# Performance work log

Measured on AMD Instinct MI355X. Metric: run time of the kernel, lower is better.

## Reference

```python
import jax, jax.numpy as jnp
import numpy as np

B, C, H, W = 64, 2048, 14, 14
D, S, ITERS, EPS, HID = 256, 8, 3, 1e-8, 512


def build_pos(h, w, d):
    gy, gx = np.meshgrid(np.arange(h), np.arange(w), indexing='ij')
    q = d // 4
    omega = 1.0 / (10000.0 ** (np.arange(q) / q))
    ey = gy.reshape(-1, 1) * omega
    ex = gx.reshape(-1, 1) * omega
    pe = np.concatenate([np.sin(ey), np.cos(ey), np.sin(ex), np.cos(ex)], axis=1)
    return jnp.asarray(pe[None], jnp.float32)  # (1, h*w, d)


def layernorm(x, g, b, eps=1e-5):
    m = x.mean(-1, keepdims=True)
    v = ((x - m) ** 2).mean(-1, keepdims=True)
    return (x - m) * jax.lax.rsqrt(v + eps) * g + b


def setup_inputs() -> dict:
    key = jax.random.key(0)
    ks = jax.random.split(key, 16)
    w = lambda k, shp, s=0.02: jax.random.normal(k, shp, jnp.float32) * s
    inp = {
        'x': jax.random.normal(ks[0], (B, C, H, W), jnp.float32),
        'slot_noise': jax.random.normal(ks[1], (B, S, D), jnp.float32),
        'conv_w': w(ks[2], (C, D)), 'conv_b': jnp.zeros((D,), jnp.float32),
        'pos': build_pos(H, W, D),
        'slots_mu': jax.random.normal(ks[3], (1, 1, D), jnp.float32),
        'slots_logsigma': -jnp.ones((1, 1, D), jnp.float32),
        'qw': w(ks[4], (D, D)), 'qb': jnp.zeros((D,), jnp.float32),
        'kw': w(ks[5], (D, D)), 'kb': jnp.zeros((D,), jnp.float32),
        'vw': w(ks[6], (D, D)), 'vb': jnp.zeros((D,), jnp.float32),
        'gru_wih': w(ks[7], (D, 3 * D)), 'gru_whh': w(ks[8], (D, 3 * D)),
        'gru_bih': jnp.zeros((3 * D,), jnp.float32), 'gru_bhh': jnp.zeros((3 * D,), jnp.float32),
        'w1': w(ks[9], (D, HID)), 'b1': jnp.zeros((HID,), jnp.float32),
        'w2': w(ks[10], (HID, D)), 'b2': jnp.zeros((D,), jnp.float32),
        'ln_in_g': jnp.ones((D,), jnp.float32), 'ln_in_b': jnp.zeros((D,), jnp.float32),
        'ln_s_g': jnp.ones((D,), jnp.float32), 'ln_s_b': jnp.zeros((D,), jnp.float32),
        'ln_ff_g': jnp.ones((D,), jnp.float32), 'ln_ff_b': jnp.zeros((D,), jnp.float32),
    }
    return inp


def reference(x, slot_noise, conv_w, conv_b, pos, slots_mu, slots_logsigma,
              qw, qb, kw, kb, vw, vb, gru_wih, gru_whh, gru_bih, gru_bhh,
              w1, b1, w2, b2, ln_in_g, ln_in_b, ln_s_g, ln_s_b, ln_ff_g, ln_ff_b):
    b, c, h, w_ = x.shape
    d = qw.shape[0]
    scale = d ** (-0.5)
    # (B,C,H,W) -> (B,N,C) -> project -> add pos
    xt = x.transpose(0, 2, 3, 1).reshape(b, h * w_, c)
    xt = xt @ conv_w + conv_b + pos
    # slot init
    slots = slots_mu + jnp.exp(slots_logsigma) * slot_noise  # (B,S,D)
    inp = layernorm(xt, ln_in_g, ln_in_b)
    k = inp @ kw + kb
    v = inp @ vw + vb
    attn = None
    for _ in range(ITERS):
        slots_prev = slots
        s = layernorm(slots, ln_s_g, ln_s_b)
        q = s @ qw + qb
        dots = jnp.einsum('bid,bjd->bij', q, k) * scale  # (B,S,N)
        attn = jax.nn.softmax(dots, axis=1) + EPS  # softmax over slots
        attn = attn / attn.sum(-1, keepdims=True)  # renormalize over keys
        updates = jnp.einsum('bjd,bij->bid', v, attn)  # (B,S,D)
        # GRUCell (torch semantics)
        gi = updates @ gru_wih + gru_bih
        gh = slots_prev @ gru_whh + gru_bhh
        ir, iz, inn = jnp.split(gi, 3, axis=-1)
        hr, hz, hn = jnp.split(gh, 3, axis=-1)
        r = jax.nn.sigmoid(ir + hr)
        z = jax.nn.sigmoid(iz + hz)
        nn_ = jnp.tanh(inn + r * hn)
        slots = (1.0 - z) * nn_ + z * slots_prev
        ff = layernorm(slots, ln_ff_g, ln_ff_b)
        slots = slots + (jax.nn.relu(ff @ w1 + b1)) @ w2 + b2
    attn_map = attn.reshape(b, S, h, w_)
    return slots, attn_map
```

## Files before the change

kernel.cpp:

```cpp
#include <hip/hip_runtime.h>
#include <stdint.h>

#define HWN 196
#define CIN 2048
#define DD  256
#define BB  64
#define NSLOT 8
#define KVPAD 224
#define MTOT 12544

typedef __attribute__((ext_vector_type(8))) short short8;
typedef __attribute__((ext_vector_type(4))) float f32x4;
typedef __attribute__((ext_vector_type(4))) unsigned short us4;

__device__ __forceinline__ ushort f2bf(float f){ union{float f;uint32_t u;}v;v.f=f;uint32_t u=v.u;return (ushort)((u+0x7FFFu+((u>>16)&1u))>>16);}
__device__ __forceinline__ float bf2f(ushort h){ union{uint32_t u;float f;}v;v.u=((uint32_t)h)<<16;return v.f;}
__device__ __forceinline__ float sigm(float x){ return 1.f/(1.f+expf(-x)); }

__device__ __forceinline__ short8 ldsY(const ushort* buf, int LD, int kt, int lane){
    int row = lane & 15;
    int ch = kt*4 + (lane>>4);
    return *(const short8*)&buf[row*LD + ((ch ^ (row&7))<<3)];
}
__device__ __forceinline__ short8 gX(const ushort* base, int K, int nrow, int kt, int lane){
    return *(const short8*)&base[(size_t)nrow*K + kt*32 + (lane>>4)*8];
}

struct TD { const float* s; ushort* d; int R, C, t0; };
struct TD8 { TD a[8]; };

__global__ __launch_bounds__(256) void k_prep(TD8 td){
    __shared__ float tile[32][33];
    int bt = blockIdx.x;
    int mi = 0;
    #pragma unroll
    for (int i = 1; i < 8; ++i) if (bt >= td.a[i].t0) mi = i;
    TD d = td.a[mi];
    int lt = bt - d.t0;
    int tilesx = (d.C + 31) >> 5;
    int cb = (lt % tilesx) * 32, rb = (lt / tilesx) * 32;
    int tx = threadIdx.x & 31, ty = threadIdx.x >> 5;
    for (int i = ty; i < 32; i += 8) {
        int r = rb + i, c = cb + tx;
        tile[i][tx] = (r < d.R && c < d.C) ? d.s[(size_t)r * d.C + c] : 0.f;
    }
    __syncthreads();
    for (int i = ty; i < 32; i += 8) {
        int c = cb + i, r = rb + tx;
        if (c < d.C && r < d.R) d.d[(size_t)c * d.R + r] = f2bf(tile[tx][i]);
    }
}

__global__ __launch_bounds__(256) void k_proj(const float* __restrict__ x,
        const ushort* __restrict__ bT, const float* __restrict__ cb,
        const float* __restrict__ pos, ushort* __restrict__ xt){
    __shared__ ushort As[64 * 64];
    __shared__ ushort Bs[128 * 64];
    const int t = threadIdx.x;
    const int lane = t & 63;
    const int wv = t >> 6;
    const int wm = wv >> 1, wn = wv & 1;
    int mtile, nh;
    {
        int bid = blockIdx.x;
        if (bid < 384){
            int c = bid & 7, nhb = (bid >> 3) & 1, g = bid >> 4;
            mtile = g*8 + c; nh = nhb;
        } else {
            int lin = bid - 384;
            mtile = 192 + (lin >> 1); nh = lin & 1;
        }
    }
    const int bm = mtile * 64;
    const int bn = nh * 128;

    const int am = t & 63;
    const int mg = bm + am;
    const int ab = mg / HWN, ap = mg % HWN;
    const float* aptr = x + (size_t)ab * (CIN * HWN) + ap;
    const int achb = t >> 6;

    const int bnl = t >> 1;
    const int bch0 = (t & 1) * 4;
    const ushort* bptr = bT + (size_t)(bn + bnl) * CIN;

    f32x4 acc[2][4] = {};

    for (int k0 = 0; k0 < CIN; k0 += 64) {
        if (k0) __syncthreads();
        #pragma unroll
        for (int p = 0; p < 2; ++p) {
            int ch = achb + 4 * p;
            short8 av;
            #pragma unroll
            for (int j = 0; j < 8; ++j)
                av[j] = (short)f2bf(aptr[(size_t)(k0 + ch * 8 + j) * HWN]);
            *(short8*)&As[am * 64 + ((ch ^ (am & 7)) << 3)] = av;
        }
        #pragma unroll
        for (int c = 0; c < 4; ++c) {
            int ch = bch0 + c;
            short8 bv = *(const short8*)&bptr[k0 + ch * 8];
            *(short8*)&Bs[bnl * 64 + ((ch ^ (bnl & 7)) << 3)] = bv;
        }
        __syncthreads();
        #pragma unroll
        for (int kk = 0; kk < 2; ++kk) {
            short8 afr[2], bfr[4];
            #pragma unroll
            for (int mi = 0; mi < 2; ++mi) {
                int row = wm * 32 + mi * 16 + (lane & 15);
                int ch = kk * 4 + (lane >> 4);
                afr[mi] = *(const short8*)&As[row * 64 + ((ch ^ (row & 7)) << 3)];
            }
            #pragma unroll
            for (int ni = 0; ni < 4; ++ni) {
                int row = wn * 64 + ni * 16 + (lane & 15);
                int ch = kk * 4 + (lane >> 4);
                bfr[ni] = *(const short8*)&Bs[row * 64 + ((ch ^ (row & 7)) << 3)];
            }
            #pragma unroll
            for (int mi = 0; mi < 2; ++mi)
                #pragma unroll
                for (int ni = 0; ni < 4; ++ni)
                    acc[mi][ni] = __builtin_amdgcn_mfma_f32_16x16x32_bf16(
                        afr[mi], bfr[ni], acc[mi][ni], 0, 0, 0);
        }
    }
    #pragma unroll
    for (int mi = 0; mi < 2; ++mi) {
        #pragma unroll
        for (int ni = 0; ni < 4; ++ni) {
            int n = bn + wn * 64 + ni * 16 + (lane & 15);
            float cbn = cb[n];
            #pragma unroll
            for (int r = 0; r < 4; ++r) {
                int row = wm * 32 + mi * 16 + (lane >> 4) * 4 + r;
                int m = bm + row;
                int p = m % HWN;
                xt[(size_t)m * DD + n] = f2bf(acc[mi][ni][r] + cbn + pos[(size_t)p * DD + n]);
            }
        }
    }
}

__global__ __launch_bounds__(512) void k_kvinit(const ushort* __restrict__ xt,
        const ushort* __restrict__ kwT, const ushort* __restrict__ vwT,
        const float* __restrict__ kb, const float* __restrict__ vb,
        const float* __restrict__ lng, const float* __restrict__ lnb,
        ushort* __restrict__ kbf, ushort* __restrict__ vT,
        const float* __restrict__ noise, const float* __restrict__ mu,
        const float* __restrict__ lsig,
        const ushort* __restrict__ qwT, const float* __restrict__ qb,
        const float* __restrict__ gs, const float* __restrict__ bs,
        float* __restrict__ slots, ushort* __restrict__ qbuf){
    __shared__ ushort As[32*256];
    __shared__ float Sld[16*256];
    __shared__ float part[8][16][2];
    __shared__ float stats[16][2];
    const int t = threadIdx.x, lane = t & 63, wv = t >> 6;
    if (blockIdx.x < 448){
        const int b = blockIdx.x / 7, pblk = blockIdx.x % 7;
        {
            int row = t >> 4, seg = t & 15;
            int grow = b*HWN + pblk*32 + row;
            if (grow > MTOT-1) grow = MTOT-1;
            const ushort* src = &xt[(size_t)grow*DD + seg*16];
            short8 v0 = *(const short8*)&src[0];
            short8 v1 = *(const short8*)&src[8];
            float f[16];
            #pragma unroll
            for (int j = 0; j < 8; ++j){ f[j] = bf2f((ushort)v0[j]); f[8+j] = bf2f((ushort)v1[j]); }
            float s = 0.f, sq = 0.f;
            #pragma unroll
            for (int j = 0; j < 16; ++j){ s += f[j]; sq += f[j]*f[j]; }
            #pragma unroll
            for (int m = 8; m >= 1; m >>= 1){ s += __shfl_xor(s, m, 64); sq += __shfl_xor(sq, m, 64); }
            float mean = s * (1.f/256.f);
            float rs = rsqrtf(sq*(1.f/256.f) - mean*mean + 1e-5f);
            int d0 = seg*16;
            short8 o0, o1;
            #pragma unroll
            for (int j = 0; j < 8; ++j){
                o0[j] = (short)f2bf((f[j]   - mean)*rs*lng[d0+j]   + lnb[d0+j]);
                o1[j] = (short)f2bf((f[8+j] - mean)*rs*lng[d0+8+j] + lnb[d0+8+j]);
            }
            int ch0 = seg*2;
            *(short8*)&As[row*256 + ((ch0^(row&7))<<3)] = o0;
            *(short8*)&As[row*256 + (((ch0+1)^(row&7))<<3)] = o1;
        }
        __syncthreads();
        f32x4 acck[2][2] = {}, accv[2][2] = {};
        const int n0 = wv*32;
        #pragma unroll
        for (int kt = 0; kt < 8; ++kt){
            short8 afr[2];
            #pragma unroll
            for (int mi = 0; mi < 2; ++mi){
                int row = mi*16 + (lane&15);
                int ch = kt*4 + (lane>>4);
                afr[mi] = *(const short8*)&As[row*256 + ((ch^(row&7))<<3)];
            }
            #pragma unroll
            for (int ni = 0; ni < 2; ++ni){
                int n = n0 + ni*16 + (lane&15);
                int koff = kt*32 + (lane>>4)*8;
                short8 bk = *(const short8*)&kwT[(size_t)n*DD + koff];
                short8 bv = *(const short8*)&vwT[(size_t)n*DD + koff];
                #pragma unroll
                for (int mi = 0; mi < 2; ++mi){
                    acck[mi][ni] = __builtin_amdgcn_mfma_f32_16x16x32_bf16(afr[mi], bk, acck[mi][ni],0,0,0);
                    accv[mi][ni] = __builtin_amdgcn_mfma_f32_16x16x32_bf16(afr[mi], bv, accv[mi][ni],0,0,0);
                }
            }
        }
        #pragma unroll
        for (int mi = 0; mi < 2; ++mi){
            #pragma unroll
            for (int ni = 0; ni < 2; ++ni){
                int n = n0 + ni*16 + (lane&15);
                float kbn = kb[n], vbn = vb[n];
                int pl0 = pblk*32 + mi*16 + (lane>>4)*4;
                us4 pk;
                #pragma unroll
                for (int r = 0; r < 4; ++r){
                    kbf[((size_t)b*KVPAD + pl0 + r)*DD + n] = f2bf(acck[mi][ni][r] + kbn);
                    pk[r] = f2bf(accv[mi][ni][r] + vbn);
                }
                *(us4*)&vT[((size_t)b*DD + n)*KVPAD + pl0] = pk;
            }
        }
    } else {
        ushort* Ysn = As;
        const int bb = blockIdx.x - 448, rbase = bb*16;
        const int w = wv;
        {
            int row = t>>5, ch = t&31; int d = ch*8;
            f32x4 n0 = *(const f32x4*)&noise[(size_t)(rbase+row)*DD + d];
            f32x4 n1 = *(const f32x4*)&noise[(size_t)(rbase+row)*DD + d + 4];
            f32x4 m0 = *(const f32x4*)&mu[d];
            f32x4 m1 = *(const f32x4*)&mu[d+4];
            f32x4 l0 = *(const f32x4*)&lsig[d];
            f32x4 l1 = *(const f32x4*)&lsig[d+4];
            f32x4 s0, s1;
            #pragma unroll
            for (int j = 0; j < 4; ++j){
                s0[j] = m0[j] + expf(l0[j])*n0[j];
                s1[j] = m1[j] + expf(l1[j])*n1[j];
            }
            *(f32x4*)&slots[(size_t)(rbase+row)*DD + d] = s0;
            *(f32x4*)&slots[(size_t)(rbase+row)*DD + d + 4] = s1;
            *(f32x4*)&Sld[row*256 + d] = s0;
            *(f32x4*)&Sld[row*256 + d + 4] = s1;
        }
        __syncthreads();
        f32x4 sv[2];
        #pragma unroll
        for (int sub = 0; sub < 2; ++sub){
            int d0 = w*32 + sub*16 + (lane>>4)*4;
            sv[sub] = *(const f32x4*)&Sld[(lane&15)*256 + d0];
        }
        {
            float lsum = 0.f, lsq = 0.f;
            #pragma unroll
            for (int sub = 0; sub < 2; ++sub)
                #pragma unroll
                for (int r = 0; r < 4; ++r){ float v = sv[sub][r]; lsum += v; lsq += v*v; }
            lsum += __shfl_xor(lsum, 16, 64); lsum += __shfl_xor(lsum, 32, 64);
            lsq  += __shfl_xor(lsq, 16, 64);  lsq  += __shfl_xor(lsq, 32, 64);
            if (lane < 16){ part[w][lane][0] = lsum; part[w][lane][1] = lsq; }
        }
        __syncthreads();
        if (t < 16){
            float a = 0.f, c = 0.f;
            #pragma unroll
            for (int i = 0; i < 8; ++i){ a += part[i][t][0]; c += part[i][t][1]; }
            float mean = a*(1.f/256.f);
            stats[t][0] = mean;
            stats[t][1] = rsqrtf(c*(1.f/256.f) - mean*mean + 1e-5f);
        }
        __syncthreads();
        {
            int slot = lane&15;
            float mean = stats[slot][0], rs = stats[slot][1];
            #pragma unroll
            for (int sub = 0; sub < 2; ++sub){
                int d0 = w*32 + sub*16 + (lane>>4)*4;
                f32x4 g4 = *(const f32x4*)&gs[d0];
                f32x4 b4 = *(const f32x4*)&bs[d0];
                us4 o;
                #pragma unroll
                for (int r = 0; r < 4; ++r) o[r] = f2bf((sv[sub][r]-mean)*rs*g4[r] + b4[r]);
                int ch = d0>>3;
                *(us4*)&Ysn[slot*256 + ((ch^(slot&7))<<3) + (d0&7)] = o;
            }
        }
        __syncthreads();
        f32x4 qa[2] = {};
        #pragma unroll
        for (int kt = 0; kt < 8; ++kt){
            short8 ysn = ldsY(Ysn, 256, kt, lane);
            #pragma unroll
            for (int sub = 0; sub < 2; ++sub){
                int nrow = w*32 + sub*16 + (lane&15);
                short8 xx = gX(qwT, 256, nrow, kt, lane);
                qa[sub] = __builtin_amdgcn_mfma_f32_16x16x32_bf16(xx, ysn, qa[sub], 0,0,0);
            }
        }
        #pragma unroll
        for (int sub = 0; sub < 2; ++sub){
            int qd0 = w*32 + sub*16 + (lane>>4)*4;
            f32x4 qb4 = *(const f32x4*)&qb[qd0];
            us4 o;
            #pragma unroll
            for (int r = 0; r < 4; ++r) o[r] = f2bf((qa[sub][r]+qb4[r])*0.0625f);
            *(us4*)&qbuf[(size_t)(rbase+(lane&15))*DD + qd0] = o;
        }
    }
}

__device__ __forceinline__ float sm_ep(f32x4 acc, int f, int lane, ushort* Xat, int srow){
    int k0 = f*16 + (lane>>4)*4;
    us4 o;
    float ps = 0.f;
    #pragma unroll
    for (int r = 0; r < 4; ++r){
        float v = acc[r];
        float mx = v;
        mx = fmaxf(mx, __shfl_xor(mx, 1, 64));
        mx = fmaxf(mx, __shfl_xor(mx, 2, 64));
        mx = fmaxf(mx, __shfl_xor(mx, 4, 64));
        float e = expf(v - mx);
        float se = e;
        se += __shfl_xor(se, 1, 64);
        se += __shfl_xor(se, 2, 64);
        se += __shfl_xor(se, 4, 64);
        float val = e/se + 1e-8f;
        if (k0 + r >= HWN) val = 0.f;
        ps += val;
        o[r] = f2bf(val);
    }
    int ch = k0 >> 3;
    *(us4*)&Xat[srow*256 + ((ch^(srow&7))<<3) + (k0&7)] = o;
    return ps;
}

__global__ __launch_bounds__(1024, 2) void k_slot(
        const ushort* __restrict__ qbuf, const ushort* __restrict__ kbf,
        const ushort* __restrict__ vT, float* __restrict__ slots,
        ushort* __restrict__ qout,
        const ushort* __restrict__ wihT, const ushort* __restrict__ whhT,
        const float* __restrict__ bih, const float* __restrict__ bhh,
        const ushort* __restrict__ w1T, const float* __restrict__ b1,
        const ushort* __restrict__ w2T, const float* __restrict__ b2,
        const float* __restrict__ gff, const float* __restrict__ bff,
        const float* __restrict__ gs, const float* __restrict__ bs,
        const ushort* __restrict__ qwT, const float* __restrict__ qb,
        float* __restrict__ out_slots, float* __restrict__ out_attn,
        int final_){
    __shared__ ushort Yq[16*256];
    __shared__ ushort Xat[16*256];
    __shared__ ushort Yupd[16*256];
    __shared__ ushort Yslb[16*256];
    __shared__ ushort Ysn[16*256];
    __shared__ ushort Yh[16*512];
    __shared__ float wpart[16][16];
    __shared__ float part[16][16][2];
    const int t = threadIdx.x, lane = t & 63, w = t >> 6;
    const int b = blockIdx.x;
    const int rbase = b * NSLOT;
    const int srow = lane & 15;
    const int srd = (srow < NSLOT) ? srow : 0;

    if (t < 256){
        int row = t>>5, ch = t&31;
        short8 v = *(const short8*)&qbuf[(size_t)(rbase+row)*DD + ch*8];
        *(short8*)&Yq[row*256 + ((ch^(row&7))<<3)] = v;
        f32x4 s0 = *(const f32x4*)&slots[(size_t)(rbase+row)*DD + ch*8];
        f32x4 s1 = *(const f32x4*)&slots[(size_t)(rbase+row)*DD + ch*8 + 4];
        short8 sv;
        #pragma unroll
        for (int j = 0; j < 4; ++j){ sv[j] = (short)f2bf(s0[j]); sv[4+j] = (short)f2bf(s1[j]); }
        *(short8*)&Yslb[row*256 + ((ch^(row&7))<<3)] = sv;
    } else if (t < 512){
        int i = t - 256;
        int row = (i>>5) + 8, ch = i&31;
        short8 z;
        #pragma unroll
        for (int j = 0; j < 8; ++j) z[j] = 0;
        *(short8*)&Yq[row*256 + ((ch^(row&7))<<3)] = z;
        *(short8*)&Yupd[row*256 + ((ch^(row&7))<<3)] = z;
        *(short8*)&Yslb[row*256 + ((ch^(row&7))<<3)] = z;
    }
    __syncthreads();
    if (w < 14){
        short8 yf[8];
        #pragma unroll
        for (int kt = 0; kt < 8; ++kt) yf[kt] = ldsY(Yq, 256, kt, lane);
        const ushort* kb_ = kbf + (size_t)b*KVPAD*DD;
        const int r0 = w*16 + (lane&15);
        short8 xa[2];
        xa[0] = gX(kb_, 256, r0, 0, lane);
        f32x4 accA = {};
        #pragma unroll
        for (int kt = 0; kt < 8; ++kt){
            int cu = kt & 1, nx = cu ^ 1;
            if (kt < 7) xa[nx] = gX(kb_, 256, r0, kt+1, lane);
            accA = __builtin_amdgcn_mfma_f32_16x16x32_bf16(xa[cu], yf[kt], accA, 0,0,0);
        }
        float ps = sm_ep(accA, w, lane, Xat, srow);
        ps += __shfl_xor(ps, 16, 64);
        ps += __shfl_xor(ps, 32, 64);
        if (lane < 16) wpart[w][lane] = ps;
    } else {
        if (lane < 16) wpart[w][lane] = 0.f;
    }
    __syncthreads();
    f32x4 pv;
    {
        short8 xat[7];
        #pragma unroll
        for (int kt = 0; kt < 7; ++kt) xat[kt] = ldsY(Xat, 256, kt, lane);
        const ushort* vb_ = vT + (size_t)b*DD*KVPAD;
        const int d0r = w*16 + (lane&15);
        short8 ya[2];
        ya[0] = gX(vb_, KVPAD, d0r, 0, lane);
        f32x4 aA = {};
        #pragma unroll
        for (int kt = 0; kt < 7; ++kt){
            int cu = kt & 1, nx = cu ^ 1;
            if (kt < 6) ya[nx] = gX(vb_, KVPAD, d0r, kt+1, lane);
            aA = __builtin_amdgcn_mfma_f32_16x16x32_bf16(xat[kt], ya[cu], aA, 0,0,0);
        }
        pv = aA;
    }
    {
        f32x4 iv;
        #pragma unroll
        for (int r = 0; r < 4; ++r){
            int s2 = (lane>>4)*4 + r;
            float s = 0.f;
            #pragma unroll
            for (int i = 0; i < 16; ++i) s += wpart[i][s2];
            iv[r] = 1.f/s;
        }
        int d0 = w*16;
        #pragma unroll
        for (int r = 0; r < 4; ++r){
            int s2 = (lane>>4)*4 + r;
            if (s2 < NSLOT){
                int d = d0 + (lane&15);
                int ch = d >> 3;
                Yupd[s2*256 + ((ch^(s2&7))<<3) + (d&7)] = f2bf(pv[r]*iv[r]);
            }
        }
    }
    if (final_){
        for (int idx = t; idx < NSLOT*HWN; idx += 1024){
            int slot = idx/HWN, key = idx - slot*HWN;
            float s = 0.f;
            #pragma unroll
            for (int i = 0; i < 16; ++i) s += wpart[i][slot];
            int ch = key >> 3;
            out_attn[(size_t)b*NSLOT*HWN + idx] =
                bf2f(Xat[slot*256 + ((ch^(slot&7))<<3) + (key&7)]) / s;
        }
    }
    __syncthreads();
    f32x4 gi[3] = {}, gh[3] = {};
    {
        int nrw[3];
        #pragma unroll
        for (int g = 0; g < 3; ++g) nrw[g] = g*256 + w*16 + (lane&15);
        short8 xw[2][6];
        #pragma unroll
        for (int g = 0; g < 3; ++g){
            xw[0][g]   = gX(wihT, 256, nrw[g], 0, lane);
            xw[0][3+g] = gX(whhT, 256, nrw[g], 0, lane);
        }
        #pragma unroll
        for (int kt = 0; kt < 8; ++kt){
            int cu = kt & 1, nx = cu ^ 1;
            if (kt < 7){
                #pragma unroll
                for (int g = 0; g < 3; ++g){
                    xw[nx][g]   = gX(wihT, 256, nrw[g], kt+1, lane);
                    xw[nx][3+g] = gX(whhT, 256, nrw[g], kt+1, lane);
                }
            }
            short8 yu = ldsY(Yupd, 256, kt, lane);
            short8 ys = ldsY(Yslb, 256, kt, lane);
            #pragma unroll
            for (int g = 0; g < 3; ++g){
                gi[g] = __builtin_amdgcn_mfma_f32_16x16x32_bf16(xw[cu][g],   yu, gi[g], 0,0,0);
                gh[g] = __builtin_amdgcn_mfma_f32_16x16x32_bf16(xw[cu][3+g], ys, gh[g], 0,0,0);
            }
        }
    }
    f32x4 snew;
    {
        int d0 = w*16 + (lane>>4)*4;
        f32x4 sp  = *(const f32x4*)&slots[(size_t)(rbase + srd)*DD + d0];
        f32x4 bir = *(const f32x4*)&bih[d0];
        f32x4 biz = *(const f32x4*)&bih[256 + d0];
        f32x4 bin = *(const f32x4*)&bih[512 + d0];
        f32x4 bhr = *(const f32x4*)&bhh[d0];
        f32x4 bhz = *(const f32x4*)&bhh[256 + d0];
        f32x4 bhn = *(const f32x4*)&bhh[512 + d0];
        #pragma unroll
        for (int r = 0; r < 4; ++r){
            float ir = gi[0][r] + bir[r];
            float iz = gi[1][r] + biz[r];
            float in_ = gi[2][r] + bin[r];
            float hr = gh[0][r] + bhr[r];
            float hz = gh[1][r] + bhz[r];
            float hn = gh[2][r] + bhn[r];
            float rr = sigm(ir + hr);
            float zz = sigm(iz + hz);
            float nn = tanhf(in_ + rr*hn);
            snew[r] = (1.f - zz)*nn + zz*sp[r];
        }
    }
    {
        float lsum = 0.f, lsq = 0.f;
        #pragma unroll
        for (int r = 0; r < 4; ++r){ float v = snew[r]; lsum += v; lsq += v*v; }
        lsum += __shfl_xor(lsum, 16, 64); lsum += __shfl_xor(lsum, 32, 64);
        lsq  += __shfl_xor(lsq, 16, 64);  lsq  += __shfl_xor(lsq, 32, 64);
        if (lane < 16){ part[w][lane][0] = lsum; part[w][lane][1] = lsq; }
    }
    __syncthreads();
    {
        float a = 0.f, c = 0.f;
        #pragma unroll
        for (int i = 0; i < 16; ++i){ a += part[i][srow][0]; c += part[i][srow][1]; }
        float mean = a*(1.f/256.f);
        float rs = rsqrtf(c*(1.f/256.f) - mean*mean + 1e-5f);
        int d0 = w*16 + (lane>>4)*4;
        f32x4 g4 = *(const f32x4*)&gff[d0];
        f32x4 b4 = *(const f32x4*)&bff[d0];
        us4 o;
        #pragma unroll
        for (int r = 0; r < 4; ++r) o[r] = f2bf((snew[r]-mean)*rs*g4[r] + b4[r]);
        int ch = d0 >> 3;
        *(us4*)&Ysn[srow*256 + ((ch^(srow&7))<<3) + (d0&7)] = o;
    }
    __syncthreads();
    {
        int nr1[2];
        #pragma unroll
        for (int s2 = 0; s2 < 2; ++s2) nr1[s2] = w*32 + s2*16 + (lane&15);
        short8 xw1[2][2];
        #pragma unroll
        for (int s2 = 0; s2 < 2; ++s2) xw1[0][s2] = gX(w1T, 256, nr1[s2], 0, lane);
        f32x4 hh[2] = {};
        #pragma unroll
        for (int kt = 0; kt < 8; ++kt){
            int cu = kt & 1, nx = cu ^ 1;
            if (kt < 7){
                #pragma unroll
                for (int s2 = 0; s2 < 2; ++s2) xw1[nx][s2] = gX(w1T, 256, nr1[s2], kt+1, lane);
            }
            short8 ysn = ldsY(Ysn, 256, kt, lane);
            #pragma unroll
            for (int s2 = 0; s2 < 2; ++s2)
                hh[s2] = __builtin_amdgcn_mfma_f32_16x16x32_bf16(xw1[cu][s2], ysn, hh[s2], 0,0,0);
        }
        #pragma unroll
        for (int s2 = 0; s2 < 2; ++s2){
            int n0 = w*32 + s2*16 + (lane>>4)*4;
            f32x4 b14 = *(const f32x4*)&b1[n0];
            us4 o;
            #pragma unroll
            for (int r = 0; r < 4; ++r) o[r] = f2bf(fmaxf(hh[s2][r] + b14[r], 0.f));
            int ch = n0 >> 3;
            *(us4*)&Yh[srow*512 + ((ch^(srow&7))<<3) + (n0&7)] = o;
        }
    }
    __syncthreads();
    f32x4 ns;
    {
        int nr2 = w*16 + (lane&15);
        short8 xw2[2];
        xw2[0] = gX(w2T, 512, nr2, 0, lane);
        f32x4 o2 = {};
        #pragma unroll
        for (int kt = 0; kt < 16; ++kt){
            int cu = kt & 1, nx = cu ^ 1;
            if (kt < 15) xw2[nx] = gX(w2T, 512, nr2, kt+1, lane);
            short8 yh = ldsY(Yh, 512, kt, lane);
            o2 = __builtin_amdgcn_mfma_f32_16x16x32_bf16(xw2[cu], yh, o2, 0,0,0);
        }
        float* dst = final_ ? out_slots : slots;
        int d0 = w*16 + (lane>>4)*4;
        f32x4 b24 = *(const f32x4*)&b2[d0];
        #pragma unroll
        for (int r = 0; r < 4; ++r) ns[r] = o2[r] + b24[r] + snew[r];
        if (srow < NSLOT)
            *(f32x4*)&dst[(size_t)(rbase + srow)*DD + d0] = ns;
    }
    if (final_) return;
    {
        float lsum = 0.f, lsq = 0.f;
        #pragma unroll
        for (int r = 0; r < 4; ++r){ float v = ns[r]; lsum += v; lsq += v*v; }
        lsum += __shfl_xor(lsum, 16, 64); lsum += __shfl_xor(lsum, 32, 64);
        lsq  += __shfl_xor(lsq, 16, 64);  lsq  += __shfl_xor(lsq, 32, 64);
        if (lane < 16){ part[w][lane][0] = lsum; part[w][lane][1] = lsq; }
    }
    __syncthreads();
    {
        float a = 0.f, c = 0.f;
        #pragma unroll
        for (int i = 0; i < 16; ++i){ a += part[i][srow][0]; c += part[i][srow][1]; }
        float mean = a*(1.f/256.f);
        float rs = rsqrtf(c*(1.f/256.f) - mean*mean + 1e-5f);
        int d0 = w*16 + (lane>>4)*4;
        f32x4 g4 = *(const f32x4*)&gs[d0];
        f32x4 b4 = *(const f32x4*)&bs[d0];
        us4 o;
        #pragma unroll
        for (int r = 0; r < 4; ++r) o[r] = f2bf((ns[r]-mean)*rs*g4[r] + b4[r]);
        int ch = d0 >> 3;
        *(us4*)&Ysn[srow*256 + ((ch^(srow&7))<<3) + (d0&7)] = o;
    }
    __syncthreads();
    {
        int nrq = w*16 + (lane&15);
        short8 xq[2];
        xq[0] = gX(qwT, 256, nrq, 0, lane);
        f32x4 qa = {};
        #pragma unroll
        for (int kt = 0; kt < 8; ++kt){
            int cu = kt & 1, nx = cu ^ 1;
            if (kt < 7) xq[nx] = gX(qwT, 256, nrq, kt+1, lane);
            short8 ysn = ldsY(Ysn, 256, kt, lane);
            qa = __builtin_amdgcn_mfma_f32_16x16x32_bf16(xq[cu], ysn, qa, 0,0,0);
        }
        int qd0 = w*16 + (lane>>4)*4;
        f32x4 qb4 = *(const f32x4*)&qb[qd0];
        us4 o;
        #pragma unroll
        for (int r = 0; r < 4; ++r) o[r] = f2bf((qa[r]+qb4[r])*0.0625f);
        if (srow < NSLOT)
            *(us4*)&qout[(size_t)(rbase + srow)*DD + qd0] = o;
    }
}

extern "C" void kernel_launch(void* const* d_in, const int* in_sizes, int n_in,
                              void* d_out, int out_size, void* d_ws, size_t ws_size,
                              hipStream_t stream) {
    const float* x      = (const float*)d_in[0];
    const float* noise  = (const float*)d_in[1];
    const float* conv_w = (const float*)d_in[2];
    const float* conv_b = (const float*)d_in[3];
    const float* pos    = (const float*)d_in[4];
    const float* mu     = (const float*)d_in[5];
    const float* logsig = (const float*)d_in[6];
    const float* qw  = (const float*)d_in[7];
    const float* qb  = (const float*)d_in[8];
    const float* kw  = (const float*)d_in[9];
    const float* kb  = (const float*)d_in[10];
    const float* vw  = (const float*)d_in[11];
    const float* vb  = (const float*)d_in[12];
    const float* wih = (const float*)d_in[13];
    const float* whh = (const float*)d_in[14];
    const float* bih = (const float*)d_in[15];
    const float* bhh = (const float*)d_in[16];
    const float* w1  = (const float*)d_in[17];
    const float* b1  = (const float*)d_in[18];
    const float* w2  = (const float*)d_in[19];
    const float* b2  = (const float*)d_in[20];
    const float* g_in = (const float*)d_in[21];
    const float* b_in = (const float*)d_in[22];
    const float* g_s  = (const float*)d_in[23];
    const float* b_s  = (const float*)d_in[24];
    const float* g_ff = (const float*)d_in[25];
    const float* b_ff = (const float*)d_in[26];

    char* w = (char*)d_ws;
    ushort* kbf    = (ushort*)w; w += (size_t)BB*KVPAD*DD*2;
    ushort* vT     = (ushort*)w; w += (size_t)BB*DD*KVPAD*2;
    ushort* cwT    = (ushort*)w; w += (size_t)DD*CIN*2;
    ushort* qwT    = (ushort*)w; w += (size_t)DD*DD*2;
    ushort* kwT    = (ushort*)w; w += (size_t)DD*DD*2;
    ushort* vwT    = (ushort*)w; w += (size_t)DD*DD*2;
    ushort* wihT   = (ushort*)w; w += (size_t)768*DD*2;
    ushort* whhT   = (ushort*)w; w += (size_t)768*DD*2;
    ushort* w1T    = (ushort*)w; w += (size_t)512*DD*2;
    ushort* w2T    = (ushort*)w; w += (size_t)DD*512*2;
    ushort* qbb    = (ushort*)w; w += (size_t)BB*NSLOT*DD*2;
    float*  slotsb = (float*)w;  w += (size_t)BB*NSLOT*DD*4;
    ushort* xt     = (ushort*)w; w += (size_t)MTOT*DD*2;

    float* out_slots = (float*)d_out;
    float* out_attn  = (float*)d_out + (size_t)BB*NSLOT*DD;

    TD8 td;
    td.a[0] = { conv_w, cwT, 2048, 256,    0 };
    td.a[1] = { qw,     qwT,  256, 256,  512 };
    td.a[2] = { kw,     kwT,  256, 256,  576 };
    td.a[3] = { vw,     vwT,  256, 256,  640 };
    td.a[4] = { wih,    wihT, 256, 768,  704 };
    td.a[5] = { whh,    whhT, 256, 768,  896 };
    td.a[6] = { w1,     w1T,  256, 512, 1088 };
    td.a[7] = { w2,     w2T,  512, 256, 1216 };

    k_prep<<<1344, 256, 0, stream>>>(td);
    k_proj<<<392, 256, 0, stream>>>(x, cwT, conv_b, pos, xt);
    k_kvinit<<<480, 512, 0, stream>>>(xt, kwT, vwT, kb, vb, g_in, b_in, kbf, vT,
                                      noise, mu, logsig, qwT, qb, g_s, b_s,
                                      slotsb, qbb);
    for (int it = 0; it < 3; ++it){
        k_slot<<<BB, 1024, 0, stream>>>(qbb, kbf, vT, slotsb, qbb,
                                        wihT, whhT, bih, bhh, w1T, b1, w2T, b2,
                                        g_ff, b_ff, g_s, b_s, qwT, qb,
                                        out_slots, out_attn, it == 2);
    }
}
```

Before: 221.6 us.

## Fuse all three slot-attention iterations into one persistent kernel

Slot initialization and the q projection move out of the kv kernel, and the three per-iteration k_slot launches become a single k_slot3 kernel. It loops over the iterations with the slot state kept in shared memory (Sl), so the global slots and q buffers are gone. This removes two kernel launches and the global round trips of slot and q state between iterations. It adds shared memory per block and more barriers, and only 64 blocks do the work, so the loss of launch-level overlap is the main risk.

```diff
diff --git a/kernel.cpp b/kernel.cpp
--- a/kernel.cpp
+++ b/kernel.cpp
@@ -144,177 +144,81 @@
     }
 }
 
-__global__ __launch_bounds__(512) void k_kvinit(const ushort* __restrict__ xt,
+__global__ __launch_bounds__(512) void k_kv(const ushort* __restrict__ xt,
         const ushort* __restrict__ kwT, const ushort* __restrict__ vwT,
         const float* __restrict__ kb, const float* __restrict__ vb,
         const float* __restrict__ lng, const float* __restrict__ lnb,
-        ushort* __restrict__ kbf, ushort* __restrict__ vT,
-        const float* __restrict__ noise, const float* __restrict__ mu,
-        const float* __restrict__ lsig,
-        const ushort* __restrict__ qwT, const float* __restrict__ qb,
-        const float* __restrict__ gs, const float* __restrict__ bs,
-        float* __restrict__ slots, ushort* __restrict__ qbuf){
+        ushort* __restrict__ kbf, ushort* __restrict__ vT){
     __shared__ ushort As[32*256];
-    __shared__ float Sld[16*256];
-    __shared__ float part[8][16][2];
-    __shared__ float stats[16][2];
     const int t = threadIdx.x, lane = t & 63, wv = t >> 6;
-    if (blockIdx.x < 448){
-        const int b = blockIdx.x / 7, pblk = blockIdx.x % 7;
-        {
-            int row = t >> 4, seg = t & 15;
-            int grow = b*HWN + pblk*32 + row;
-            if (grow > MTOT-1) grow = MTOT-1;
-            const ushort* src = &xt[(size_t)grow*DD + seg*16];
-            short8 v0 = *(const short8*)&src[0];
-            short8 v1 = *(const short8*)&src[8];
-            float f[16];
-            #pragma unroll
-            for (int j = 0; j < 8; ++j){ f[j] = bf2f((ushort)v0[j]); f[8+j] = bf2f((ushort)v1[j]); }
-            float s = 0.f, sq = 0.f;
-            #pragma unroll
-            for (int j = 0; j < 16; ++j){ s += f[j]; sq += f[j]*f[j]; }
-            #pragma unroll
-            for (int m = 8; m >= 1; m >>= 1){ s += __shfl_xor(s, m, 64); sq += __shfl_xor(sq, m, 64); }
-            float mean = s * (1.f/256.f);
-            float rs = rsqrtf(sq*(1.f/256.f) - mean*mean + 1e-5f);
-            int d0 = seg*16;
-            short8 o0, o1;
-            #pragma unroll
-            for (int j = 0; j < 8; ++j){
-                o0[j] = (short)f2bf((f[j]   - mean)*rs*lng[d0+j]   + lnb[d0+j]);
-                o1[j] = (short)f2bf((f[8+j] - mean)*rs*lng[d0+8+j] + lnb[d0+8+j]);
-            }
-            int ch0 = seg*2;
-            *(short8*)&As[row*256 + ((ch0^(row&7))<<3)] = o0;
-            *(short8*)&As[row*256 + (((ch0+1)^(row&7))<<3)] = o1;
-        }
-        __syncthreads();
-        f32x4 acck[2][2] = {}, accv[2][2] = {};
-        const int n0 = wv*32;
-        #pragma unroll
-        for (int kt = 0; kt < 8; ++kt){
-            short8 afr[2];
+    const int b = blockIdx.x / 7, pblk = blockIdx.x % 7;
+    {
+        int row = t >> 4, seg = t & 15;
+        int grow = b*HWN + pblk*32 + row;
+        if (grow > MTOT-1) grow = MTOT-1;
+        const ushort* src = &xt[(size_t)grow*DD + seg*16];
+        short8 v0 = *(const short8*)&src[0];
+        short8 v1 = *(const short8*)&src[8];
+        float f[16];
+        #pragma unroll
+        for (int j = 0; j < 8; ++j){ f[j] = bf2f((ushort)v0[j]); f[8+j] = bf2f((ushort)v1[j]); }
+        float s = 0.f, sq = 0.f;
+        #pragma unroll
+        for (int j = 0; j < 16; ++j){ s += f[j]; sq += f[j]*f[j]; }
+        #pragma unroll
+        for (int m = 8; m >= 1; m >>= 1){ s += __shfl_xor(s, m, 64); sq += __shfl_xor(sq, m, 64); }
+        float mean = s * (1.f/256.f);
+        float rs = rsqrtf(sq*(1.f/256.f) - mean*mean + 1e-5f);
+        int d0 = seg*16;
+        short8 o0, o1;
+        #pragma unroll
+        for (int j = 0; j < 8; ++j){
+            o0[j] = (short)f2bf((f[j]   - mean)*rs*lng[d0+j]   + lnb[d0+j]);
+            o1[j] = (short)f2bf((f[8+j] - mean)*rs*lng[d0+8+j] + lnb[d0+8+j]);
+        }
+        int ch0 = seg*2;
+        *(short8*)&As[row*256 + ((ch0^(row&7))<<3)] = o0;
+        *(short8*)&As[row*256 + (((ch0+1)^(row&7))<<3)] = o1;
+    }
+    __syncthreads();
+    f32x4 acck[2][2] = {}, accv[2][2] = {};
+    const int n0 = wv*32;
+    #pragma unroll
+    for (int kt = 0; kt < 8; ++kt){
+        short8 afr[2];
+        #pragma unroll
+        for (int mi = 0; mi < 2; ++mi){
+            int row = mi*16 + (lane&15);
+            int ch = kt*4 + (lane>>4);
+            afr[mi] = *(const short8*)&As[row*256 + ((ch^(row&7))<<3)];
+        }
+        #pragma unroll
+        for (int ni = 0; ni < 2; ++ni){
+            int n = n0 + ni*16 + (lane&15);
+            int koff = kt*32 + (lane>>4)*8;
+            short8 bk = *(const short8*)&kwT[(size_t)n*DD + koff];
+            short8 bv = *(const short8*)&vwT[(size_t)n*DD + koff];
             #pragma unroll
             for (int mi = 0; mi < 2; ++mi){
-                int row = mi*16 + (lane&15);
-                int ch = kt*4 + (lane>>4);
-                afr[mi] = *(const short8*)&As[row*256 + ((ch^(row&7))<<3)];
-            }
-            #pragma unroll
-            for (int ni = 0; ni < 2; ++ni){
-                int n = n0 + ni*16 + (lane&15);
-                int koff = kt*32 + (lane>>4)*8;
-                short8 bk = *(const short8*)&kwT[(size_t)n*DD + koff];
-                short8 bv = *(const short8*)&vwT[(size_t)n*DD + koff];
-                #pragma unroll
-                for (int mi = 0; mi < 2; ++mi){
-                    acck[mi][ni] = __builtin_amdgcn_mfma_f32_16x16x32_bf16(afr[mi], bk, acck[mi][ni],0,0,0);
-                    accv[mi][ni] = __builtin_amdgcn_mfma_f32_16x16x32_bf16(afr[mi], bv, accv[mi][ni],0,0,0);
-                }
-            }
-        }
-        #pragma unroll
-        for (int mi = 0; mi < 2; ++mi){
-            #pragma unroll
-            for (int ni = 0; ni < 2; ++ni){
-                int n = n0 + ni*16 + (lane&15);
-                float kbn = kb[n], vbn = vb[n];
-                int pl0 = pblk*32 + mi*16 + (lane>>4)*4;
-                us4 pk;
-                #pragma unroll
-                for (int r = 0; r < 4; ++r){
-                    kbf[((size_t)b*KVPAD + pl0 + r)*DD + n] = f2bf(acck[mi][ni][r] + kbn);
-                    pk[r] = f2bf(accv[mi][ni][r] + vbn);
-                }
-                *(us4*)&vT[((size_t)b*DD + n)*KVPAD + pl0] = pk;
-            }
-        }
-    } else {
-        ushort* Ysn = As;
-        const int bb = blockIdx.x - 448, rbase = bb*16;
-        const int w = wv;
-        {
-            int row = t>>5, ch = t&31; int d = ch*8;
-            f32x4 n0 = *(const f32x4*)&noise[(size_t)(rbase+row)*DD + d];
-            f32x4 n1 = *(const f32x4*)&noise[(size_t)(rbase+row)*DD + d + 4];
-            f32x4 m0 = *(const f32x4*)&mu[d];
-            f32x4 m1 = *(const f32x4*)&mu[d+4];
-            f32x4 l0 = *(const f32x4*)&lsig[d];
-            f32x4 l1 = *(const f32x4*)&lsig[d+4];
-            f32x4 s0, s1;
-            #pragma unroll
-            for (int j = 0; j < 4; ++j){
-                s0[j] = m0[j] + expf(l0[j])*n0[j];
-                s1[j] = m1[j] + expf(l1[j])*n1[j];
-            }
-            *(f32x4*)&slots[(size_t)(rbase+row)*DD + d] = s0;
-            *(f32x4*)&slots[(size_t)(rbase+row)*DD + d + 4] = s1;
-            *(f32x4*)&Sld[row*256 + d] = s0;
-            *(f32x4*)&Sld[row*256 + d + 4] = s1;
-        }
-        __syncthreads();
-        f32x4 sv[2];
-        #pragma unroll
-        for (int sub = 0; sub < 2; ++sub){
-            int d0 = w*32 + sub*16 + (lane>>4)*4;
-            sv[sub] = *(const f32x4*)&Sld[(lane&15)*256 + d0];
-        }
-        {
-            float lsum = 0.f, lsq = 0.f;
-            #pragma unroll
-            for (int sub = 0; sub < 2; ++sub)
-                #pragma unroll
-                for (int r = 0; r < 4; ++r){ float v = sv[sub][r]; lsum += v; lsq += v*v; }
-            lsum += __shfl_xor(lsum, 16, 64); lsum += __shfl_xor(lsum, 32, 64);
-            lsq  += __shfl_xor(lsq, 16, 64);  lsq  += __shfl_xor(lsq, 32, 64);
-            if (lane < 16){ part[w][lane][0] = lsum; part[w][lane][1] = lsq; }
-        }
-        __syncthreads();
-        if (t < 16){
-            float a = 0.f, c = 0.f;
-            #pragma unroll
-            for (int i = 0; i < 8; ++i){ a += part[i][t][0]; c += part[i][t][1]; }
-            float mean = a*(1.f/256.f);
-            stats[t][0] = mean;
-            stats[t][1] = rsqrtf(c*(1.f/256.f) - mean*mean + 1e-5f);
-        }
-        __syncthreads();
-        {
-            int slot = lane&15;
-            float mean = stats[slot][0], rs = stats[slot][1];
-            #pragma unroll
-            for (int sub = 0; sub < 2; ++sub){
-                int d0 = w*32 + sub*16 + (lane>>4)*4;
-                f32x4 g4 = *(const f32x4*)&gs[d0];
-                f32x4 b4 = *(const f32x4*)&bs[d0];
-                us4 o;
-                #pragma unroll
-                for (int r = 0; r < 4; ++r) o[r] = f2bf((sv[sub][r]-mean)*rs*g4[r] + b4[r]);
-                int ch = d0>>3;
-                *(us4*)&Ysn[slot*256 + ((ch^(slot&7))<<3) + (d0&7)] = o;
-            }
-        }
-        __syncthreads();
-        f32x4 qa[2] = {};
-        #pragma unroll
-        for (int kt = 0; kt < 8; ++kt){
-            short8 ysn = ldsY(Ysn, 256, kt, lane);
-            #pragma unroll
-            for (int sub = 0; sub < 2; ++sub){
-                int nrow = w*32 + sub*16 + (lane&15);
-                short8 xx = gX(qwT, 256, nrow, kt, lane);
-                qa[sub] = __builtin_amdgcn_mfma_f32_16x16x32_bf16(xx, ysn, qa[sub], 0,0,0);
-            }
-        }
-        #pragma unroll
-        for (int sub = 0; sub < 2; ++sub){
-            int qd0 = w*32 + sub*16 + (lane>>4)*4;
-            f32x4 qb4 = *(const f32x4*)&qb[qd0];
-            us4 o;
-            #pragma unroll
-            for (int r = 0; r < 4; ++r) o[r] = f2bf((qa[sub][r]+qb4[r])*0.0625f);
-            *(us4*)&qbuf[(size_t)(rbase+(lane&15))*DD + qd0] = o;
+                acck[mi][ni] = __builtin_amdgcn_mfma_f32_16x16x32_bf16(afr[mi], bk, acck[mi][ni],0,0,0);
+                accv[mi][ni] = __builtin_amdgcn_mfma_f32_16x16x32_bf16(afr[mi], bv, accv[mi][ni],0,0,0);
+            }
+        }
+    }
+    #pragma unroll
+    for (int mi = 0; mi < 2; ++mi){
+        #pragma unroll
+        for (int ni = 0; ni < 2; ++ni){
+            int n = n0 + ni*16 + (lane&15);
+            float kbn = kb[n], vbn = vb[n];
+            int pl0 = pblk*32 + mi*16 + (lane>>4)*4;
+            us4 pk;
+            #pragma unroll
+            for (int r = 0; r < 4; ++r){
+                kbf[((size_t)b*KVPAD + pl0 + r)*DD + n] = f2bf(acck[mi][ni][r] + kbn);
+                pk[r] = f2bf(accv[mi][ni][r] + vbn);
+            }
+            *(us4*)&vT[((size_t)b*DD + n)*KVPAD + pl0] = pk;
         }
     }
 }
@@ -345,25 +249,25 @@
     return ps;
 }
 
-__global__ __launch_bounds__(1024, 2) void k_slot(
-        const ushort* __restrict__ qbuf, const ushort* __restrict__ kbf,
-        const ushort* __restrict__ vT, float* __restrict__ slots,
-        ushort* __restrict__ qout,
+__global__ __launch_bounds__(1024, 2) void k_slot3(
+        const float* __restrict__ noise, const float* __restrict__ mu,
+        const float* __restrict__ lsig,
+        const ushort* __restrict__ qwT, const float* __restrict__ qb,
+        const ushort* __restrict__ kbf, const ushort* __restrict__ vT,
         const ushort* __restrict__ wihT, const ushort* __restrict__ whhT,
         const float* __restrict__ bih, const float* __restrict__ bhh,
         const ushort* __restrict__ w1T, const float* __restrict__ b1,
         const ushort* __restrict__ w2T, const float* __restrict__ b2,
         const float* __restrict__ gff, const float* __restrict__ bff,
         const float* __restrict__ gs, const float* __restrict__ bs,
-        const ushort* __restrict__ qwT, const float* __restrict__ qb,
-        float* __restrict__ out_slots, float* __restrict__ out_attn,
-        int final_){
+        float* __restrict__ out_slots, float* __restrict__ out_attn){
     __shared__ ushort Yq[16*256];
     __shared__ ushort Xat[16*256];
     __shared__ ushort Yupd[16*256];
     __shared__ ushort Yslb[16*256];
     __shared__ ushort Ysn[16*256];
     __shared__ ushort Yh[16*512];
+    __shared__ float Sl[8*256];
     __shared__ float wpart[16][16];
     __shared__ float part[16][16][2];
     const int t = threadIdx.x, lane = t & 63, w = t >> 6;
@@ -372,17 +276,7 @@
     const int srow = lane & 15;
     const int srd = (srow < NSLOT) ? srow : 0;
 
-    if (t < 256){
-        int row = t>>5, ch = t&31;
-        short8 v = *(const short8*)&qbuf[(size_t)(rbase+row)*DD + ch*8];
-        *(short8*)&Yq[row*256 + ((ch^(row&7))<<3)] = v;
-        f32x4 s0 = *(const f32x4*)&slots[(size_t)(rbase+row)*DD + ch*8];
-        f32x4 s1 = *(const f32x4*)&slots[(size_t)(rbase+row)*DD + ch*8 + 4];
-        short8 sv;
-        #pragma unroll
-        for (int j = 0; j < 4; ++j){ sv[j] = (short)f2bf(s0[j]); sv[4+j] = (short)f2bf(s1[j]); }
-        *(short8*)&Yslb[row*256 + ((ch^(row&7))<<3)] = sv;
-    } else if (t < 512){
+    if (t >= 256 && t < 512){
         int i = t - 256;
         int row = (i>>5) + 8, ch = i&31;
         short8 z;
@@ -392,258 +286,286 @@
         *(short8*)&Yupd[row*256 + ((ch^(row&7))<<3)] = z;
         *(short8*)&Yslb[row*256 + ((ch^(row&7))<<3)] = z;
     }
+    if (t < 512){
+        int idx = t*4;
+        int row = idx >> 8, d = idx & 255;
+        f32x4 nz = *(const f32x4*)&noise[((size_t)rbase+row)*DD + d];
+        f32x4 o;
+        #pragma unroll
+        for (int j = 0; j < 4; ++j) o[j] = mu[d+j] + expf(lsig[d+j])*nz[j];
+        *(f32x4*)&Sl[idx] = o;
+    }
     __syncthreads();
-    if (w < 14){
-        short8 yf[8];
-        #pragma unroll
-        for (int kt = 0; kt < 8; ++kt) yf[kt] = ldsY(Yq, 256, kt, lane);
-        const ushort* kb_ = kbf + (size_t)b*KVPAD*DD;
-        const int r0 = w*16 + (lane&15);
-        short8 xa[2];
-        xa[0] = gX(kb_, 256, r0, 0, lane);
-        f32x4 accA = {};
-        #pragma unroll
-        for (int kt = 0; kt < 8; ++kt){
-            int cu = kt & 1, nx = cu ^ 1;
-            if (kt < 7) xa[nx] = gX(kb_, 256, r0, kt+1, lane);
-            accA = __builtin_amdgcn_mfma_f32_16x16x32_bf16(xa[cu], yf[kt], accA, 0,0,0);
-        }
-        float ps = sm_ep(accA, w, lane, Xat, srow);
-        ps += __shfl_xor(ps, 16, 64);
-        ps += __shfl_xor(ps, 32, 64);
-        if (lane < 16) wpart[w][lane] = ps;
-    } else {
-        if (lane < 16) wpart[w][lane] = 0.f;
-    }
-    __syncthreads();
-    f32x4 pv;
-    {
-        short8 xat[7];
-        #pragma unroll
-        for (int kt = 0; kt < 7; ++kt) xat[kt] = ldsY(Xat, 256, kt, lane);
-        const ushort* vb_ = vT + (size_t)b*DD*KVPAD;
-        const int d0r = w*16 + (lane&15);
-        short8 ya[2];
-        ya[0] = gX(vb_, KVPAD, d0r, 0, lane);
-        f32x4 aA = {};
-        #pragma unroll
-        for (int kt = 0; kt < 7; ++kt){
-            int cu = kt & 1, nx = cu ^ 1;
-            if (kt < 6) ya[nx] = gX(vb_, KVPAD, d0r, kt+1, lane);
-            aA = __builtin_amdgcn_mfma_f32_16x16x32_bf16(xat[kt], ya[cu], aA, 0,0,0);
-        }
-        pv = aA;
-    }
-    {
-        f32x4 iv;
-        #pragma unroll
-        for (int r = 0; r < 4; ++r){
-            int s2 = (lane>>4)*4 + r;
-            float s = 0.f;
-            #pragma unroll
-            for (int i = 0; i < 16; ++i) s += wpart[i][s2];
-            iv[r] = 1.f/s;
-        }
-        int d0 = w*16;
-        #pragma unroll
-        for (int r = 0; r < 4; ++r){
-            int s2 = (lane>>4)*4 + r;
-            if (s2 < NSLOT){
-                int d = d0 + (lane&15);
-                int ch = d >> 3;
-                Yupd[s2*256 + ((ch^(s2&7))<<3) + (d&7)] = f2bf(pv[r]*iv[r]);
-            }
-        }
-    }
-    if (final_){
-        for (int idx = t; idx < NSLOT*HWN; idx += 1024){
-            int slot = idx/HWN, key = idx - slot*HWN;
-            float s = 0.f;
-            #pragma unroll
-            for (int i = 0; i < 16; ++i) s += wpart[i][slot];
-            int ch = key >> 3;
-            out_attn[(size_t)b*NSLOT*HWN + idx] =
-                bf2f(Xat[slot*256 + ((ch^(slot&7))<<3) + (key&7)]) / s;
-        }
-    }
-    __syncthreads();
-    f32x4 gi[3] = {}, gh[3] = {};
-    {
-        int nrw[3];
-        #pragma unroll
-        for (int g = 0; g < 3; ++g) nrw[g] = g*256 + w*16 + (lane&15);
-        short8 xw[2][6];
-        #pragma unroll
-        for (int g = 0; g < 3; ++g){
-            xw[0][g]   = gX(wihT, 256, nrw[g], 0, lane);
-            xw[0][3+g] = gX(whhT, 256, nrw[g], 0, lane);
-        }
-        #pragma unroll
-        for (int kt = 0; kt < 8; ++kt){
-            int cu = kt & 1, nx = cu ^ 1;
-            if (kt < 7){
+
+    for (int it = 0; it < 3; ++it){
+        if (t < 256){
+            int row = t>>5, ch = t&31;
+            f32x4 s0 = *(const f32x4*)&Sl[row*256 + ch*8];
+            f32x4 s1 = *(const f32x4*)&Sl[row*256 + ch*8 + 4];
+            short8 sv;
+            #pragma unroll
+            for (int j = 0; j < 4; ++j){ sv[j] = (short)f2bf(s0[j]); sv[4+j] = (short)f2bf(s1[j]); }
+            *(short8*)&Yslb[row*256 + ((ch^(row&7))<<3)] = sv;
+        }
+        f32x4 sv_;
+        {
+            int d0 = w*16 + (lane>>4)*4;
+            sv_ = *(const f32x4*)&Sl[srd*256 + d0];
+            float lsum = 0.f, lsq = 0.f;
+            #pragma unroll
+            for (int r = 0; r < 4; ++r){ float v = sv_[r]; lsum += v; lsq += v*v; }
+            lsum += __shfl_xor(lsum, 16, 64); lsum += __shfl_xor(lsum, 32, 64);
+            lsq  += __shfl_xor(lsq, 16, 64);  lsq  += __shfl_xor(lsq, 32, 64);
+            if (lane < 16){ part[w][lane][0] = lsum; part[w][lane][1] = lsq; }
+        }
+        __syncthreads();
+        {
+            float a = 0.f, c = 0.f;
+            #pragma unroll
+            for (int i = 0; i < 16; ++i){ a += part[i][srow][0]; c += part[i][srow][1]; }
+            float mean = a*(1.f/256.f);
+            float rs = rsqrtf(c*(1.f/256.f) - mean*mean + 1e-5f);
+            int d0 = w*16 + (lane>>4)*4;
+            f32x4 g4 = *(const f32x4*)&gs[d0];
+            f32x4 b4 = *(const f32x4*)&bs[d0];
+            us4 o;
+            #pragma unroll
+            for (int r = 0; r < 4; ++r) o[r] = f2bf((sv_[r]-mean)*rs*g4[r] + b4[r]);
+            int ch = d0 >> 3;
+            *(us4*)&Ysn[srow*256 + ((ch^(srow&7))<<3) + (d0&7)] = o;
+        }
+        __syncthreads();
+        {
+            int nrq = w*16 + (lane&15);
+            short8 xq[2];
+            xq[0] = gX(qwT, 256, nrq, 0, lane);
+            f32x4 qa = {};
+            #pragma unroll
+            for (int kt = 0; kt < 8; ++kt){
+                int cu = kt & 1, nx = cu ^ 1;
+                if (kt < 7) xq[nx] = gX(qwT, 256, nrq, kt+1, lane);
+                short8 ysn = ldsY(Ysn, 256, kt, lane);
+                qa = __builtin_amdgcn_mfma_f32_16x16x32_bf16(xq[cu], ysn, qa, 0,0,0);
+            }
+            int qd0 = w*16 + (lane>>4)*4;
+            f32x4 qb4 = *(const f32x4*)&qb[qd0];
+            us4 o;
+            #pragma unroll
+            for (int r = 0; r < 4; ++r) o[r] = f2bf((qa[r]+qb4[r])*0.0625f);
+            if (srow < NSLOT){
+                int ch = qd0 >> 3;
+                *(us4*)&Yq[srow*256 + ((ch^(srow&7))<<3) + (qd0&7)] = o;
+            }
+        }
+        __syncthreads();
+        if (w < 14){
+            short8 yf[8];
+            #pragma unroll
+            for (int kt = 0; kt < 8; ++kt) yf[kt] = ldsY(Yq, 256, kt, lane);
+            const ushort* kb_ = kbf + (size_t)b*KVPAD*DD;
+            const int r0 = w*16 + (lane&15);
+            short8 xa[2];
+            xa[0] = gX(kb_, 256, r0, 0, lane);
+            f32x4 accA = {};
+            #pragma unroll
+            for (int kt = 0; kt < 8; ++kt){
+                int cu = kt & 1, nx = cu ^ 1;
+                if (kt < 7) xa[nx] = gX(kb_, 256, r0, kt+1, lane);
+                accA = __builtin_amdgcn_mfma_f32_16x16x32_bf16(xa[cu], yf[kt], accA, 0,0,0);
+            }
+            float ps = sm_ep(accA, w, lane, Xat, srow);
+            ps += __shfl_xor(ps, 16, 64);
+            ps += __shfl_xor(ps, 32, 64);
+            if (lane < 16) wpart[w][lane] = ps;
+        } else {
+            if (lane < 16) wpart[w][lane] = 0.f;
+        }
+        __syncthreads();
+        f32x4 pv;
+        {
+            short8 xat[7];
+            #pragma unroll
+            for (int kt = 0; kt < 7; ++kt) xat[kt] = ldsY(Xat, 256, kt, lane);
+            const ushort* vb_ = vT + (size_t)b*DD*KVPAD;
+            const int d0r = w*16 + (lane&15);
+            short8 ya[2];
+            ya[0] = gX(vb_, KVPAD, d0r, 0, lane);
+            f32x4 aA = {};
+            #pragma unroll
+            for (int kt = 0; kt < 7; ++kt){
+                int cu = kt & 1, nx = cu ^ 1;
+                if (kt < 6) ya[nx] = gX(vb_, KVPAD, d0r, kt+1, lane);
+                aA = __builtin_amdgcn_mfma_f32_16x16x32_bf16(xat[kt], ya[cu], aA, 0,0,0);
+            }
+            pv = aA;
+        }
+        {
+            f32x4 iv;
+            #pragma unroll
+            for (int r = 0; r < 4; ++r){
+                int s2 = (lane>>4)*4 + r;
+                float s = 0.f;
+                #pragma unroll
+                for (int i = 0; i < 16; ++i) s += wpart[i][s2];
+                iv[r] = 1.f/s;
+            }
+            int d0 = w*16;
+            #pragma unroll
+            for (int r = 0; r < 4; ++r){
+                int s2 = (lane>>4)*4 + r;
+                if (s2 < NSLOT){
+                    int d = d0 + (lane&15);
+                    int ch = d >> 3;
+                    Yupd[s2*256 + ((ch^(s2&7))<<3) + (d&7)] = f2bf(pv[r]*iv[r]);
+                }
+            }
+        }
+        if (it == 2){
+            for (int idx = t; idx < NSLOT*HWN; idx += 1024){
+                int slot = idx/HWN, key = idx - slot*HWN;
+                float s = 0.f;
+                #pragma unroll
+                for (int i = 0; i < 16; ++i) s += wpart[i][slot];
+                int ch = key >> 3;
+                out_attn[(size_t)b*NSLOT*HWN + idx] =
+                    bf2f(Xat[slot*256 + ((ch^(slot&7))<<3) + (key&7)]) / s;
+            }
+        }
+        __syncthreads();
+        f32x4 gi[3] = {}, gh[3] = {};
+        {
+            int nrw[3];
+            #pragma unroll
+            for (int g = 0; g < 3; ++g) nrw[g] = g*256 + w*16 + (lane&15);
+            short8 xw[2][6];
+            #pragma unroll
+            for (int g = 0; g < 3; ++g){
+                xw[0][g]   = gX(wihT, 256, nrw[g], 0, lane);
+                xw[0][3+g] = gX(whhT, 256, nrw[g], 0, lane);
+            }
+            #pragma unroll
+            for (int kt = 0; kt < 8; ++kt){
+                int cu = kt & 1, nx = cu ^ 1;
+                if (kt < 7){
+                    #pragma unroll
+                    for (int g = 0; g < 3; ++g){
+                        xw[nx][g]   = gX(wihT, 256, nrw[g], kt+1, lane);
+                        xw[nx][3+g] = gX(whhT, 256, nrw[g], kt+1, lane);
+                    }
+                }
+                short8 yu = ldsY(Yupd, 256, kt, lane);
+                short8 ys = ldsY(Yslb, 256, kt, lane);
                 #pragma unroll
                 for (int g = 0; g < 3; ++g){
-                    xw[nx][g]   = gX(wihT, 256, nrw[g], kt+1, lane);
-                    xw[nx][3+g] = gX(whhT, 256, nrw[g], kt+1, lane);
+                    gi[g] = __builtin_amdgcn_mfma_f32_16x16x32_bf16(xw[cu][g],   yu, gi[g], 0,0,0);
+                    gh[g] = __builtin_amdgcn_mfma_f32_16x16x32_bf16(xw[cu][3+g], ys, gh[g], 0,0,0);
                 }
             }
-            short8 yu = ldsY(Yupd, 256, kt, lane);
-            short8 ys = ldsY(Yslb, 256, kt, lane);
-            #pragma unroll
-            for (int g = 0; g < 3; ++g){
-                gi[g] = __builtin_amdgcn_mfma_f32_16x16x32_bf16(xw[cu][g],   yu, gi[g], 0,0,0);
-                gh[g] = __builtin_amdgcn_mfma_f32_16x16x32_bf16(xw[cu][3+g], ys, gh[g], 0,0,0);
-            }
-        }
-    }
-    f32x4 snew;
-    {
-        int d0 = w*16 + (lane>>4)*4;
-        f32x4 sp  = *(const f32x4*)&slots[(size_t)(rbase + srd)*DD + d0];
-        f32x4 bir = *(const f32x4*)&bih[d0];
-        f32x4 biz = *(const f32x4*)&bih[256 + d0];
-        f32x4 bin = *(const f32x4*)&bih[512 + d0];
-        f32x4 bhr = *(const f32x4*)&bhh[d0];
-        f32x4 bhz = *(const f32x4*)&bhh[256 + d0];
-        f32x4 bhn = *(const f32x4*)&bhh[512 + d0];
-        #pragma unroll
-        for (int r = 0; r < 4; ++r){
-            float ir = gi[0][r] + bir[r];
-            float iz = gi[1][r] + biz[r];
-            float in_ = gi[2][r] + bin[r];
-            float hr = gh[0][r] + bhr[r];
-            float hz = gh[1][r] + bhz[r];
-            float hn = gh[2][r] + bhn[r];
-            float rr = sigm(ir + hr);
-            float zz = sigm(iz + hz);
-            float nn = tanhf(in_ + rr*hn);
-            snew[r] = (1.f - zz)*nn + zz*sp[r];
-        }
-    }
-    {
-        float lsum = 0.f, lsq = 0.f;
-        #pragma unroll
-        for (int r = 0; r < 4; ++r){ float v = snew[r]; lsum += v; lsq += v*v; }
-        lsum += __shfl_xor(lsum, 16, 64); lsum += __shfl_xor(lsum, 32, 64);
-        lsq  += __shfl_xor(lsq, 16, 64);  lsq  += __shfl_xor(lsq, 32, 64);
-        if (lane < 16){ part[w][lane][0] = lsum; part[w][lane][1] = lsq; }
-    }
-    __syncthreads();
-    {
-        float a = 0.f, c = 0.f;
-        #pragma unroll
-        for (int i = 0; i < 16; ++i){ a += part[i][srow][0]; c += part[i][srow][1]; }
-        float mean = a*(1.f/256.f);
-        float rs = rsqrtf(c*(1.f/256.f) - mean*mean + 1e-5f);
-        int d0 = w*16 + (lane>>4)*4;
-        f32x4 g4 = *(const f32x4*)&gff[d0];
-        f32x4 b4 = *(const f32x4*)&bff[d0];
-        us4 o;
-        #pragma unroll
-        for (int r = 0; r < 4; ++r) o[r] = f2bf((snew[r]-mean)*rs*g4[r] + b4[r]);
-        int ch = d0 >> 3;
-        *(us4*)&Ysn[srow*256 + ((ch^(srow&7))<<3) + (d0&7)] = o;
-    }
-    __syncthreads();
-    {
-        int nr1[2];
-        #pragma unroll
-        for (int s2 = 0; s2 < 2; ++s2) nr1[s2] = w*32 + s2*16 + (lane&15);
-        short8 xw1[2][2];
-        #pragma unroll
-        for (int s2 = 0; s2 < 2; ++s2) xw1[0][s2] = gX(w1T, 256, nr1[s2], 0, lane);
-        f32x4 hh[2] = {};
-        #pragma unroll
-        for (int kt = 0; kt < 8; ++kt){
-            int cu = kt & 1, nx = cu ^ 1;
-            if (kt < 7){
+        }
+        f32x4 snew;
+        {
+            int d0 = w*16 + (lane>>4)*4;
+            f32x4 sp  = *(const f32x4*)&Sl[srd*256 + d0];
+            f32x4 bir = *(const f32x4*)&bih[d0];
+            f32x4 biz = *(const f32x4*)&bih[256 + d0];
+            f32x4 bin = *(const f32x4*)&bih[512 + d0];
+            f32x4 bhr = *(const f32x4*)&bhh[d0];
+            f32x4 bhz = *(const f32x4*)&bhh[256 + d0];
+            f32x4 bhn = *(const f32x4*)&bhh[512 + d0];
+            #pragma unroll
+            for (int r = 0; r < 4; ++r){
+                float ir = gi[0][r] + bir[r];
+                float iz = gi[1][r] + biz[r];
+                float in_ = gi[2][r] + bin[r];
+                float hr = gh[0][r] + bhr[r];
+                float hz = gh[1][r] + bhz[r];
+                float hn = gh[2][r] + bhn[r];
+                float rr = sigm(ir + hr);
+                float zz = sigm(iz + hz);
+                float nn = tanhf(in_ + rr*hn);
+                snew[r] = (1.f - zz)*nn + zz*sp[r];
+            }
+        }
+        {
+            float lsum = 0.f, lsq = 0.f;
+            #pragma unroll
+            for (int r = 0; r < 4; ++r){ float v = snew[r]; lsum += v; lsq += v*v; }
+            lsum += __shfl_xor(lsum, 16, 64); lsum += __shfl_xor(lsum, 32, 64);
+            lsq  += __shfl_xor(lsq, 16, 64);  lsq  += __shfl_xor(lsq, 32, 64);
+            if (lane < 16){ part[w][lane][0] = lsum; part[w][lane][1] = lsq; }
+        }
+        __syncthreads();
+        {
+            float a = 0.f, c = 0.f;
+            #pragma unroll
+            for (int i = 0; i < 16; ++i){ a += part[i][srow][0]; c += part[i][srow][1]; }
+            float mean = a*(1.f/256.f);
+            float rs = rsqrtf(c*(1.f/256.f) - mean*mean + 1e-5f);
+            int d0 = w*16 + (lane>>4)*4;
+            f32x4 g4 = *(const f32x4*)&gff[d0];
+            f32x4 b4 = *(const f32x4*)&bff[d0];
+            us4 o;
+            #pragma unroll
+            for (int r = 0; r < 4; ++r) o[r] = f2bf((snew[r]-mean)*rs*g4[r] + b4[r]);
+            int ch = d0 >> 3;
+            *(us4*)&Ysn[srow*256 + ((ch^(srow&7))<<3) + (d0&7)] = o;
+        }
+        __syncthreads();
+        {
+            int nr1[2];
+            #pragma unroll
+            for (int s2 = 0; s2 < 2; ++s2) nr1[s2] = w*32 + s2*16 + (lane&15);
+            short8 xw1[2][2];
+            #pragma unroll
+            for (int s2 = 0; s2 < 2; ++s2) xw1[0][s2] = gX(w1T, 256, nr1[s2], 0, lane);
+            f32x4 hh[2] = {};
+            #pragma unroll
+            for (int kt = 0; kt < 8; ++kt){
+                int cu = kt & 1, nx = cu ^ 1;
+                if (kt < 7){
+                    #pragma unroll
+                    for (int s2 = 0; s2 < 2; ++s2) xw1[nx][s2] = gX(w1T, 256, nr1[s2], kt+1, lane);
+                }
+                short8 ysn = ldsY(Ysn, 256, kt, lane);
                 #pragma unroll
-                for (int s2 = 0; s2 < 2; ++s2) xw1[nx][s2] = gX(w1T, 256, nr1[s2], kt+1, lane);
-            }
-            short8 ysn = ldsY(Ysn, 256, kt, lane);
-            #pragma unroll
-            for (int s2 = 0; s2 < 2; ++s2)
-                hh[s2] = __builtin_amdgcn_mfma_f32_16x16x32_bf16(xw1[cu][s2], ysn, hh[s2], 0,0,0);
-        }
-        #pragma unroll
-        for (int s2 = 0; s2 < 2; ++s2){
-            int n0 = w*32 + s2*16 + (lane>>4)*4;
-            f32x4 b14 = *(const f32x4*)&b1[n0];
-            us4 o;
-            #pragma unroll
-            for (int r = 0; r < 4; ++r) o[r] = f2bf(fmaxf(hh[s2][r] + b14[r], 0.f));
-            int ch = n0 >> 3;
-            *(us4*)&Yh[srow*512 + ((ch^(srow&7))<<3) + (n0&7)] = o;
-        }
-    }
-    __syncthreads();
-    f32x4 ns;
-    {
-        int nr2 = w*16 + (lane&15);
-        short8 xw2[2];
-        xw2[0] = gX(w2T, 512, nr2, 0, lane);
-        f32x4 o2 = {};
-        #pragma unroll
-        for (int kt = 0; kt < 16; ++kt){
-            int cu = kt & 1, nx = cu ^ 1;
-            if (kt < 15) xw2[nx] = gX(w2T, 512, nr2, kt+1, lane);
-            short8 yh = ldsY(Yh, 512, kt, lane);
-            o2 = __builtin_amdgcn_mfma_f32_16x16x32_bf16(xw2[cu], yh, o2, 0,0,0);
-        }
-        float* dst = final_ ? out_slots : slots;
-        int d0 = w*16 + (lane>>4)*4;
-        f32x4 b24 = *(const f32x4*)&b2[d0];
-        #pragma unroll
-        for (int r = 0; r < 4; ++r) ns[r] = o2[r] + b24[r] + snew[r];
-        if (srow < NSLOT)
-            *(f32x4*)&dst[(size_t)(rbase + srow)*DD + d0] = ns;
-    }
-    if (final_) return;
-    {
-        float lsum = 0.f, lsq = 0.f;
-        #pragma unroll
-        for (int r = 0; r < 4; ++r){ float v = ns[r]; lsum += v; lsq += v*v; }
-        lsum += __shfl_xor(lsum, 16, 64); lsum += __shfl_xor(lsum, 32, 64);
-        lsq  += __shfl_xor(lsq, 16, 64);  lsq  += __shfl_xor(lsq, 32, 64);
-        if (lane < 16){ part[w][lane][0] = lsum; part[w][lane][1] = lsq; }
-    }
-    __syncthreads();
-    {
-        float a = 0.f, c = 0.f;
-        #pragma unroll
-        for (int i = 0; i < 16; ++i){ a += part[i][srow][0]; c += part[i][srow][1]; }
-        float mean = a*(1.f/256.f);
-        float rs = rsqrtf(c*(1.f/256.f) - mean*mean + 1e-5f);
-        int d0 = w*16 + (lane>>4)*4;
-        f32x4 g4 = *(const f32x4*)&gs[d0];
-        f32x4 b4 = *(const f32x4*)&bs[d0];
-        us4 o;
-        #pragma unroll
-        for (int r = 0; r < 4; ++r) o[r] = f2bf((ns[r]-mean)*rs*g4[r] + b4[r]);
-        int ch = d0 >> 3;
-        *(us4*)&Ysn[srow*256 + ((ch^(srow&7))<<3) + (d0&7)] = o;
-    }
-    __syncthreads();
-    {
-        int nrq = w*16 + (lane&15);
-        short8 xq[2];
-        xq[0] = gX(qwT, 256, nrq, 0, lane);
-        f32x4 qa = {};
-        #pragma unroll
-        for (int kt = 0; kt < 8; ++kt){
-            int cu = kt & 1, nx = cu ^ 1;
-            if (kt < 7) xq[nx] = gX(qwT, 256, nrq, kt+1, lane);
-            short8 ysn = ldsY(Ysn, 256, kt, lane);
-            qa = __builtin_amdgcn_mfma_f32_16x16x32_bf16(xq[cu], ysn, qa, 0,0,0);
-        }
-        int qd0 = w*16 + (lane>>4)*4;
-        f32x4 qb4 = *(const f32x4*)&qb[qd0];
-        us4 o;
-        #pragma unroll
-        for (int r = 0; r < 4; ++r) o[r] = f2bf((qa[r]+qb4[r])*0.0625f);
-        if (srow < NSLOT)
-            *(us4*)&qout[(size_t)(rbase + srow)*DD + qd0] = o;
+                for (int s2 = 0; s2 < 2; ++s2)
+                    hh[s2] = __builtin_amdgcn_mfma_f32_16x16x32_bf16(xw1[cu][s2], ysn, hh[s2], 0,0,0);
+            }
+            #pragma unroll
+            for (int s2 = 0; s2 < 2; ++s2){
+                int n0 = w*32 + s2*16 + (lane>>4)*4;
+                f32x4 b14 = *(const f32x4*)&b1[n0];
+                us4 o;
+                #pragma unroll
+                for (int r = 0; r < 4; ++r) o[r] = f2bf(fmaxf(hh[s2][r] + b14[r], 0.f));
+                int ch = n0 >> 3;
+                *(us4*)&Yh[srow*512 + ((ch^(srow&7))<<3) + (n0&7)] = o;
+            }
+        }
+        __syncthreads();
+        {
+            int nr2 = w*16 + (lane&15);
+            short8 xw2[2];
+            xw2[0] = gX(w2T, 512, nr2, 0, lane);
+            f32x4 o2 = {};
+            #pragma unroll
+            for (int kt = 0; kt < 16; ++kt){
+                int cu = kt & 1, nx = cu ^ 1;
+                if (kt < 15) xw2[nx] = gX(w2T, 512, nr2, kt+1, lane);
+                short8 yh = ldsY(Yh, 512, kt, lane);
+                o2 = __builtin_amdgcn_mfma_f32_16x16x32_bf16(xw2[cu], yh, o2, 0,0,0);
+            }
+            int d0 = w*16 + (lane>>4)*4;
+            f32x4 b24 = *(const f32x4*)&b2[d0];
+            f32x4 ns;
+            #pragma unroll
+            for (int r = 0; r < 4; ++r) ns[r] = o2[r] + b24[r] + snew[r];
+            if (srow < NSLOT){
+                if (it == 2) *(f32x4*)&out_slots[((size_t)rbase + srow)*DD + d0] = ns;
+                else         *(f32x4*)&Sl[srow*256 + d0] = ns;
+            }
+        }
+        if (it < 2) __syncthreads();
     }
 }
 
@@ -689,8 +611,6 @@
     ushort* whhT   = (ushort*)w; w += (size_t)768*DD*2;
     ushort* w1T    = (ushort*)w; w += (size_t)512*DD*2;
     ushort* w2T    = (ushort*)w; w += (size_t)DD*512*2;
-    ushort* qbb    = (ushort*)w; w += (size_t)BB*NSLOT*DD*2;
-    float*  slotsb = (float*)w;  w += (size_t)BB*NSLOT*DD*4;
     ushort* xt     = (ushort*)w; w += (size_t)MTOT*DD*2;
 
     float* out_slots = (float*)d_out;
@@ -708,13 +628,8 @@
 
     k_prep<<<1344, 256, 0, stream>>>(td);
     k_proj<<<392, 256, 0, stream>>>(x, cwT, conv_b, pos, xt);
-    k_kvinit<<<480, 512, 0, stream>>>(xt, kwT, vwT, kb, vb, g_in, b_in, kbf, vT,
-                                      noise, mu, logsig, qwT, qb, g_s, b_s,
-                                      slotsb, qbb);
-    for (int it = 0; it < 3; ++it){
-        k_slot<<<BB, 1024, 0, stream>>>(qbb, kbf, vT, slotsb, qbb,
-                                        wihT, whhT, bih, bhh, w1T, b1, w2T, b2,
-                                        g_ff, b_ff, g_s, b_s, qwT, qb,
-                                        out_slots, out_attn, it == 2);
-    }
-}
+    k_kv<<<448, 512, 0, stream>>>(xt, kwT, vwT, kb, vb, g_in, b_in, kbf, vT);
+    k_slot3<<<BB, 1024, 0, stream>>>(noise, mu, logsig, qwT, qb, kbf, vT,
+                                     wihT, whhT, bih, bhh, w1T, b1, w2T, b2,
+                                     g_ff, b_ff, g_s, b_s, out_slots, out_attn);
+}
```

Result: slower. 344.3 us (+55.4%).
